# Kernel tuning notes

Measured on AMD Instinct MI355X. Metric: run time of the kernel, lower is better.

Reference implementation:

```python
import jax, jax.numpy as jnp
import numpy as np

D = 1024           # fusion_dim
H_MHA = 16         # fusion_heads
H_GAT = 8          # graph attention heads
GAT_DH = D // H_GAT
DIL = (1, 2, 4, 8, 16)
K = 7              # temporal_kernel_size
B, T = 8, 256


def setup_inputs() -> dict:
    key = jax.random.key(0)
    ks = jax.random.split(key, 20)

    def w(k, sh, fan):
        return jax.random.normal(k, sh, jnp.float32) * np.float32(1.0 / np.sqrt(fan))

    inp = {"features": jax.random.normal(ks[0], (B, T, D), jnp.float32)}
    for i, dil in enumerate(DIL):
        inp["conv_w%d" % i] = w(ks[1 + i], (D, D, K), D * K)   # torch Conv1d (out, in, k)
        inp["conv_b%d" % i] = jnp.zeros((D,), jnp.float32)
    inp["fp_w"] = w(ks[6], (D, 5 * D), 5 * D)                    # torch Linear (out, in)
    inp["fp_b"] = jnp.zeros((D,), jnp.float32)
    inp["ln_g"] = jnp.ones((D,), jnp.float32)
    inp["ln_b"] = jnp.zeros((D,), jnp.float32)
    inp["wq"] = w(ks[7], (D, D), D); inp["bq"] = jnp.zeros((D,), jnp.float32)
    inp["wk"] = w(ks[8], (D, D), D); inp["bk"] = jnp.zeros((D,), jnp.float32)
    inp["wv"] = w(ks[9], (D, D), D); inp["bv"] = jnp.zeros((D,), jnp.float32)
    inp["wo"] = w(ks[10], (D, D), D); inp["bo"] = jnp.zeros((D,), jnp.float32)
    inp["gat_w"] = w(ks[11], (D, D), D)
    inp["gat_b"] = jnp.zeros((D,), jnp.float32)
    # original `a` is (2*head_dim, 1) shared across heads; split into a1 (source) / a2 (target)
    inp["gat_a1"] = w(ks[12], (GAT_DH,), 2 * GAT_DH)
    inp["gat_a2"] = w(ks[13], (GAT_DH,), 2 * GAT_DH)
    return inp


def _forward(features, conv_ws, conv_bs, fp_w, fp_b, ln_g, ln_b,
             wq, bq, wk, bk, wv, bv, wo, bo, gat_w, gat_b, gat_a1, gat_a2):
    Bb, Tt, Dm = features.shape
    x = jnp.transpose(features, (0, 2, 1))                       # (B, D, T)
    feats = []
    for wgt, bias, dil in zip(conv_ws, conv_bs, DIL):
        pad = (K - 1) * dil // 2                                 # 'same' padding
        y = jax.lax.conv_general_dilated(
            x, wgt, window_strides=(1,), padding=[(pad, pad)],
            rhs_dilation=(dil,), dimension_numbers=("NCH", "OIH", "NCH"))
        feats.append(jnp.transpose(y + bias[None, :, None], (0, 2, 1)))
    ms = jnp.concatenate(feats, axis=-1)                         # (B, T, 5D)
    z = ms @ fp_w.T + fp_b                                       # (B, T, D)
    mu = jnp.mean(z, -1, keepdims=True)
    var = jnp.var(z, -1, keepdims=True)
    z = (z - mu) * jax.lax.rsqrt(var + 1e-5) * ln_g + ln_b       # LayerNorm
    z = jax.nn.gelu(z, approximate=False)
    # --- multi-head self attention (batch_first, no dropout at eval) ---
    dh = Dm // H_MHA
    q = (z @ wq.T + bq).reshape(Bb, Tt, H_MHA, dh)
    k = (z @ wk.T + bk).reshape(Bb, Tt, H_MHA, dh)
    v = (z @ wv.T + bv).reshape(Bb, Tt, H_MHA, dh)
    scores = jnp.einsum("bqhd,bkhd->bhqk", q, k) * np.float32(1.0 / np.sqrt(dh))
    attn = jax.nn.softmax(scores, axis=-1)
    ctx = jnp.einsum("bhqk,bkhd->bqhd", attn, v).reshape(Bb, Tt, Dm)
    att_out = ctx @ wo.T + bo
    # --- all-pairs graph attention over N = B*T nodes (GAT-style, a shared across heads) ---
    n = Bb * Tt
    hg = (att_out.reshape(n, Dm) @ gat_w.T + gat_b).reshape(n, H_GAT, GAT_DH)
    e1 = jnp.einsum("nhd,d->nh", hg, gat_a1)                     # a1 . h_i
    e2 = jnp.einsum("nhd,d->nh", hg, gat_a2)                     # a2 . h_j
    e = jax.nn.leaky_relu(e1[:, None, :] + e2[None, :, :], 0.2)  # (N, N, H) via broadcast
    alpha = jax.nn.softmax(e, axis=1)                            # normalize over j
    hp = jnp.einsum("ijh,jhd->ihd", alpha, hg).reshape(n, Dm)
    g = jax.nn.elu(hp).reshape(Bb, Tt, Dm)
    return g + features


def reference(features, conv_w0, conv_w1, conv_w2, conv_w3, conv_w4,
              conv_b0, conv_b1, conv_b2, conv_b3, conv_b4,
              fp_w, fp_b, ln_g, ln_b,
              wq, bq, wk, bk, wv, bv, wo, bo,
              gat_w, gat_b, gat_a1, gat_a2):
    return _forward(features,
                    (conv_w0, conv_w1, conv_w2, conv_w3, conv_w4),
                    (conv_b0, conv_b1, conv_b2, conv_b3, conv_b4),
                    fp_w, fp_b, ln_g, ln_b,
                    wq, bq, wk, bk, wv, bv, wo, bo,
                    gat_w, gat_b, gat_a1, gat_a2)
```

## Files before the change

### kernel.cpp

```cpp
#include <hip/hip_runtime.h>
#include <hip/hip_bf16.h>

typedef __bf16 bf16_t;
typedef bf16_t bf16x8 __attribute__((ext_vector_type(8)));
typedef bf16_t bf16x4v __attribute__((ext_vector_type(4)));
typedef float f32x4 __attribute__((ext_vector_type(4)));

__device__ __forceinline__ void gll16(const bf16_t* g, bf16_t* l) {
    __builtin_amdgcn_global_load_lds(
        (const __attribute__((address_space(1))) unsigned int*)g,
        (__attribute__((address_space(3))) unsigned int*)l, 16, 0, 0);
}

__global__ __launch_bounds__(256)
void cvt_f32_bf16(const float* __restrict__ in, bf16_t* __restrict__ out, int n4)
{
    int i = blockIdx.x * 256 + threadIdx.x;
    if (i < n4) {
        float4 v = ((const float4*)in)[i];
        bf16x4v o = { (bf16_t)v.x, (bf16_t)v.y, (bf16_t)v.z, (bf16_t)v.w };
        *(bf16x4v*)&out[i * 4] = o;
    }
}

__global__ __launch_bounds__(256)
void cvt_multi(const float* __restrict__ fpw, const float* __restrict__ wq,
               const float* __restrict__ wk, const float* __restrict__ wv,
               const float* __restrict__ wo, const float* __restrict__ gw,
               bf16_t* __restrict__ fpwb, bf16_t* __restrict__ wqb,
               bf16_t* __restrict__ wkb, bf16_t* __restrict__ wvb,
               bf16_t* __restrict__ wob, bf16_t* __restrict__ gwb)
{
    int id = blockIdx.x * 256 + threadIdx.x;
    const float* src; bf16_t* dst; int off;
    if (id < 1310720) { src = fpw; dst = fpwb; off = id; }
    else {
        int id3 = id - 1310720;
        int w = id3 >> 18; off = id3 & 262143;
        const float* ss[5] = {wq, wk, wv, wo, gw};
        bf16_t* dd[5] = {wqb, wkb, wvb, wob, gwb};
        src = ss[w]; dst = dd[w];
    }
    float4 v = ((const float4*)src)[off];
    bf16x4v o = { (bf16_t)v.x, (bf16_t)v.y, (bf16_t)v.z, (bf16_t)v.w };
    *(bf16x4v*)&dst[off * 4] = o;
}

__global__ __launch_bounds__(256)
void reorder_convw(const float* w0, const float* w1, const float* w2,
                   const float* w3, const float* w4, bf16_t* __restrict__ out)
{
    int gid = blockIdx.x * 256 + threadIdx.x;
    int i = gid >> 20, rem = gid & 1048575;
    int o = rem >> 10, c = rem & 1023;
    const float* ws[5] = {w0, w1, w2, w3, w4};
    const float* src = ws[i] + (size_t)o * 7168 + c * 7;
    #pragma unroll
    for (int kk = 0; kk < 7; kk++)
        out[((size_t)(i * 7 + kk) << 20) + (o << 10) + c] = (bf16_t)src[kk];
}

__global__ __launch_bounds__(256)
void gather_bias(const float* b0, const float* b1, const float* b2,
                 const float* b3, const float* b4,
                 const float* bq, const float* bk,
                 float* __restrict__ out, float* __restrict__ qkbias,
                 bf16_t* __restrict__ zp)
{
    int idx = blockIdx.x * 256 + threadIdx.x;
    if (blockIdx.x == 0 && threadIdx.x < 32) zp[threadIdx.x] = (bf16_t)0.0f;
    if (idx < 5120) {
        const float* bs[5] = {b0, b1, b2, b3, b4};
        out[idx] = bs[idx >> 10][idx & 1023];
    } else {
        int j = idx - 5120;
        qkbias[j] = (j < 1024) ? bq[j] : bk[j - 1024];
    }
}

template<bool CONV, bool OUT_BF16, bool BIAS_ROW = false, int NR = 128>
__global__ __launch_bounds__(256)
void mfma_gemm(const bf16_t* __restrict__ A, const bf16_t* __restrict__ Bw,
               const float* __restrict__ bias, void* __restrict__ outv,
               const bf16_t* __restrict__ zp,
               int Kd, int lda, int ldb, int ldo, int out_col0)
{
    constexpr int FN = NR / 32;
    __shared__ __align__(16) bf16_t As[3][NR * 32];
    __shared__ __align__(16) bf16_t Bs[3][128 * 32];
    const int t = threadIdx.x;
    const int lane = t & 63, wave = t >> 6;
    const int wn = (wave & 1) * (NR / 2), wm = (wave >> 1) * 64;
    const int q = lane >> 4, lr = lane & 15;
    const int mt = CONV ? (blockIdx.x & 7) : blockIdx.x;
    const int conv_i = CONV ? (blockIdx.x >> 3) : 0;
    const int m0 = mt * 128, n0 = blockIdx.y * NR;
    const int srow = lane >> 2, sseg = lane & 3;
    const int sw_seg = sseg ^ ((srow >> 1) & 3);
    const int slotq = (q ^ ((lr >> 1) & 3)) * 8;

    f32x4 acc[FN][4];
    #pragma unroll
    for (int a = 0; a < FN; a++)
        #pragma unroll
        for (int b = 0; b < 4; b++) acc[a][b] = (f32x4){0.f, 0.f, 0.f, 0.f};

    const int ksteps = Kd >> 5;
    const int T = CONV ? ksteps * 7 : ksteps;

    int s_tap = 0, s_k0 = 0;
    auto do_stage = [&](int bi) {
        const bf16_t* Bp = CONV ? (Bw + ((size_t)(conv_i * 7 + s_tap) << 20)) : Bw;
        const int shift = CONV ? ((s_tap - 3) << conv_i) : 0;
        #pragma unroll
        for (int p = 0; p < NR / 64; p++) {
            const int slab = p * 64 + wave * 16;
            const int rr = slab + srow;
            const bf16_t* ga;
            if (CONV) {
                int n = n0 + rr;
                int tg = (n & 255) + shift;
                ga = ((unsigned)tg < 256u)
                   ? A + (size_t)((n & ~255) + tg) * lda + s_k0 + sw_seg * 8
                   : zp + sseg * 8;
            } else {
                ga = A + (size_t)(n0 + rr) * lda + s_k0 + sw_seg * 8;
            }
            gll16(ga, &As[bi][slab * 32]);
        }
        #pragma unroll
        for (int p = 0; p < 2; p++) {
            const int slab = p * 64 + wave * 16;
            const int rr = slab + srow;
            gll16(Bp + (size_t)(m0 + rr) * ldb + s_k0 + sw_seg * 8, &Bs[bi][slab * 32]);
        }
        s_k0 += 32;
        if (CONV && s_k0 == Kd) { s_k0 = 0; s_tap++; }
    };

    do_stage(0);
    do_stage(1);

    int cur = 0;
    for (int s = 0; s < T; s++) {
        if (s + 1 < T) {
            if constexpr (NR == 128) asm volatile("s_waitcnt vmcnt(4)" ::: "memory");
            else                     asm volatile("s_waitcnt vmcnt(3)" ::: "memory");
        } else {
            asm volatile("s_waitcnt vmcnt(0)" ::: "memory");
        }
        __builtin_amdgcn_s_barrier();
        __builtin_amdgcn_sched_barrier(0);

        bf16x8 af[FN], bfv[4];
        #pragma unroll
        for (int f = 0; f < FN; f++)
            af[f] = *(bf16x8*)&As[cur][(wn + f * 16 + lr) * 32 + slotq];
        #pragma unroll
        for (int f = 0; f < 4; f++)
            bfv[f] = *(bf16x8*)&Bs[cur][(wm + f * 16 + lr) * 32 + slotq];

        int nb = cur + 2; if (nb >= 3) nb -= 3;
        if (s + 2 < T) do_stage(nb);

        __builtin_amdgcn_s_setprio(1);
        #pragma unroll
        for (int fn = 0; fn < FN; fn++)
            #pragma unroll
            for (int fm = 0; fm < 4; fm++)
                acc[fn][fm] = __builtin_amdgcn_mfma_f32_16x16x32_bf16(
                    af[fn], bfv[fm], acc[fn][fm], 0, 0, 0);
        __builtin_amdgcn_s_setprio(0);
        cur++; if (cur == 3) cur = 0;
    }

    const int oc0 = CONV ? (conv_i << 10) : out_col0;
    #pragma unroll
    for (int fn = 0; fn < FN; fn++) {
        #pragma unroll
        for (int r = 0; r < 4; r++) {
            int n = n0 + wn + fn * 16 + q * 4 + r;
            #pragma unroll
            for (int fm = 0; fm < 4; fm++) {
                int m = m0 + wm + fm * 16 + lr;
                float v = acc[fn][fm][r];
                if (bias) v += bias[BIAS_ROW ? n : (oc0 + m)];
                if (OUT_BF16)
                    ((bf16_t*)outv)[(size_t)n * ldo + oc0 + m] = (bf16_t)v;
                else
                    ((float*)outv)[(size_t)n * ldo + oc0 + m] = v;
            }
        }
    }
}

__global__ __launch_bounds__(256)
void ln_gelu(float* __restrict__ z, bf16_t* __restrict__ zb,
             const float* __restrict__ g, const float* __restrict__ b)
{
    __shared__ float r1[256], r2[256];
    const int n = blockIdx.x, t = threadIdx.x;
    float* row = z + (size_t)n * 1024;
    float x[4], s = 0.f, s2 = 0.f;
    #pragma unroll
    for (int u = 0; u < 4; u++) {
        x[u] = row[t + u * 256];
        s += x[u]; s2 += x[u] * x[u];
    }
    r1[t] = s; r2[t] = s2;
    __syncthreads();
    for (int off = 128; off > 0; off >>= 1) {
        if (t < off) { r1[t] += r1[t + off]; r2[t] += r2[t + off]; }
        __syncthreads();
    }
    const float mu  = r1[0] * (1.0f / 1024.0f);
    const float var = r2[0] * (1.0f / 1024.0f) - mu * mu;
    const float rstd = rsqrtf(var + 1e-5f);
    #pragma unroll
    for (int u = 0; u < 4; u++) {
        int c = t + u * 256;
        float y = (x[u] - mu) * rstd * g[c] + b[c];
        float gv = 0.5f * y * (1.0f + erff(y * 0.70710678118654752f));
        row[c] = gv;
        zb[(size_t)n * 1024 + c] = (bf16_t)gv;
    }
}

__global__ __launch_bounds__(256)
void attn_mfma(const bf16_t* __restrict__ qg, const bf16_t* __restrict__ kg,
               const bf16_t* __restrict__ vt, bf16_t* __restrict__ ctx)
{
    const int it = blockIdx.x, h = blockIdx.y, bb = blockIdx.z;
    const int t = threadIdx.x, lane = t & 63, wave = t >> 6;
    const int q4 = lane >> 4, lr = lane & 15;
    const size_t qkbase = (size_t)bb * 256 * 2048 + (size_t)h * 64;

    __shared__ __align__(16) bf16_t Qs[4][32 * 64];
    __shared__ __align__(16) bf16_t Ks[64 * 64];
    __shared__ __align__(16) bf16_t Vs[64 * 64];
    __shared__ __align__(16) bf16_t Ps[4][32 * 64];

    {
        const int itbase = it * 128;
        #pragma unroll
        for (int rep = 0; rep < 4; rep++) {
            int idx = rep * 256 + t;
            int rl = idx >> 3, seg = idx & 7;
            bf16x8 v = *(const bf16x8*)&qg[qkbase + (size_t)(itbase + rl) * 2048 + seg * 8];
            *(bf16x8*)&Qs[rl >> 5][(rl & 31) * 64 + ((seg ^ (rl & 7)) << 3)] = v;
        }
    }

    f32x4 o[2][4];
    float mrow[2][4], lrow[2][4];
    #pragma unroll
    for (int fn = 0; fn < 2; fn++)
        #pragma unroll
        for (int x = 0; x < 4; x++) {
            o[fn][x] = (f32x4){0.f, 0.f, 0.f, 0.f};
            mrow[fn][x] = -1e30f; lrow[fn][x] = 0.f;
        }

    for (int j0 = 0; j0 < 256; j0 += 64) {
        __syncthreads();
        #pragma unroll
        for (int rep = 0; rep < 2; rep++) {
            int idx = rep * 256 + t;
            int rl = idx >> 3, seg = idx & 7;
            bf16x8 kv = *(const bf16x8*)&kg[qkbase + (size_t)(j0 + rl) * 2048 + seg * 8];
            *(bf16x8*)&Ks[rl * 64 + ((seg ^ (rl & 7)) << 3)] = kv;
            bf16x8 vv = *(const bf16x8*)&vt[(size_t)(h * 64 + rl) * 2048 + bb * 256 + j0 + seg * 8];
            *(bf16x8*)&Vs[rl * 64 + ((seg ^ (rl & 7)) << 3)] = vv;
        }
        __syncthreads();

        f32x4 s[2][4];
        #pragma unroll
        for (int fn = 0; fn < 2; fn++)
            #pragma unroll
            for (int fm = 0; fm < 4; fm++) s[fn][fm] = (f32x4){0.f, 0.f, 0.f, 0.f};
        #pragma unroll
        for (int kk = 0; kk < 2; kk++) {
            bf16x8 aq[2], bk[4];
            #pragma unroll
            for (int fn = 0; fn < 2; fn++) {
                int row = fn * 16 + lr;
                aq[fn] = *(bf16x8*)&Qs[wave][row * 64 + (((kk * 4 + q4) ^ (row & 7)) << 3)];
            }
            #pragma unroll
            for (int fm = 0; fm < 4; fm++) {
                int row = fm * 16 + lr;
                bk[fm] = *(bf16x8*)&Ks[row * 64 + (((kk * 4 + q4) ^ (row & 7)) << 3)];
            }
            #pragma unroll
            for (int fn = 0; fn < 2; fn++)
                #pragma unroll
                for (int fm = 0; fm < 4; fm++)
                    s[fn][fm] = __builtin_amdgcn_mfma_f32_16x16x32_bf16(
                        aq[fn], bk[fm], s[fn][fm], 0, 0, 0);
        }

        #pragma unroll
        for (int fn = 0; fn < 2; fn++) {
            #pragma unroll
            for (int r = 0; r < 4; r++) {
                float sv[4];
                #pragma unroll
                for (int fm = 0; fm < 4; fm++) sv[fm] = s[fn][fm][r] * 0.125f;
                float rm = fmaxf(fmaxf(sv[0], sv[1]), fmaxf(sv[2], sv[3]));
                rm = fmaxf(rm, __shfl_xor(rm, 1));
                rm = fmaxf(rm, __shfl_xor(rm, 2));
                rm = fmaxf(rm, __shfl_xor(rm, 4));
                rm = fmaxf(rm, __shfl_xor(rm, 8));
                float mold = mrow[fn][r];
                float mnew = fmaxf(mold, rm);
                float scl = __expf(mold - mnew);
                mrow[fn][r] = mnew;
                int prow = fn * 16 + q4 * 4 + r;
                float psum = 0.f;
                #pragma unroll
                for (int fm = 0; fm < 4; fm++) {
                    float p = __expf(sv[fm] - mnew);
                    psum += p;
                    int col = fm * 16 + lr;
                    Ps[wave][prow * 64 + (col ^ ((prow & 7) << 3))] = (bf16_t)p;
                }
                psum += __shfl_xor(psum, 1);
                psum += __shfl_xor(psum, 2);
                psum += __shfl_xor(psum, 4);
                psum += __shfl_xor(psum, 8);
                lrow[fn][r] = lrow[fn][r] * scl + psum;
                #pragma unroll
                for (int fd = 0; fd < 4; fd++) o[fn][fd][r] *= scl;
            }
        }

        #pragma unroll
        for (int kk = 0; kk < 2; kk++) {
            bf16x8 ap[2], bvf[4];
            #pragma unroll
            for (int fn = 0; fn < 2; fn++) {
                int row = fn * 16 + lr;
                ap[fn] = *(bf16x8*)&Ps[wave][row * 64 + (((kk * 4 + q4) ^ (row & 7)) << 3)];
            }
            #pragma unroll
            for (int fd = 0; fd < 4; fd++) {
                int row = fd * 16 + lr;
                bvf[fd] = *(bf16x8*)&Vs[row * 64 + (((kk * 4 + q4) ^ (row & 7)) << 3)];
            }
            #pragma unroll
            for (int fn = 0; fn < 2; fn++)
                #pragma unroll
                for (int fd = 0; fd < 4; fd++)
                    o[fn][fd] = __builtin_amdgcn_mfma_f32_16x16x32_bf16(
                        ap[fn], bvf[fd], o[fn][fd], 0, 0, 0);
        }
    }

    const int i0 = it * 128 + wave * 32;
    #pragma unroll
    for (int fn = 0; fn < 2; fn++) {
        #pragma unroll
        for (int r = 0; r < 4; r++) {
            float inv = 1.0f / lrow[fn][r];
            int row = i0 + fn * 16 + q4 * 4 + r;
            #pragma unroll
            for (int fd = 0; fd < 4; fd++) {
                int col = h * 64 + fd * 16 + lr;
                ctx[(size_t)bb * 262144 + (size_t)row * 1024 + col] =
                    (bf16_t)(o[fn][fd][r] * inv);
            }
        }
    }
}

__global__ __launch_bounds__(256)
void gat_e(const float* __restrict__ hg, const float* __restrict__ a1,
           const float* __restrict__ a2, float* __restrict__ e1t,
           float* __restrict__ e2t)
{
    int id = blockIdx.x * 256 + threadIdx.x;
    int h = id >> 11, n = id & 2047;
    const float* hr = hg + (size_t)n * 1024 + h * 128;
    float s1 = 0.f, s2 = 0.f;
    for (int d = 0; d < 128; d += 4) {
        float4 x = *(const float4*)&hr[d];
        float4 u1 = *(const float4*)&a1[d];
        float4 u2 = *(const float4*)&a2[d];
        s1 += x.x * u1.x + x.y * u1.y + x.z * u1.z + x.w * u1.w;
        s2 += x.x * u2.x + x.y * u2.y + x.z * u2.z + x.w * u2.w;
    }
    e1t[id] = s1; e2t[id] = s2;
}

__global__ __launch_bounds__(256)
void transpose_hg(const float* __restrict__ in, bf16_t* __restrict__ out)
{
    __shared__ float tile[32][33];
    const int t = threadIdx.x;
    const int j0 = blockIdx.x * 32, c0 = blockIdx.y * 32;
    {
        int jl = t >> 3, cl = (t & 7) * 4;
        float4 v = *(const float4*)(in + (size_t)(j0 + jl) * 1024 + c0 + cl);
        tile[jl][cl] = v.x; tile[jl][cl + 1] = v.y;
        tile[jl][cl + 2] = v.z; tile[jl][cl + 3] = v.w;
    }
    __syncthreads();
    {
        int cl = t >> 3, jl = (t & 7) * 4;
        bf16x4v o = { (bf16_t)tile[jl][cl], (bf16_t)tile[jl + 1][cl],
                      (bf16_t)tile[jl + 2][cl], (bf16_t)tile[jl + 3][cl] };
        *(bf16x4v*)&out[(size_t)(c0 + cl) * 2048 + j0 + jl] = o;
    }
}

__global__ __launch_bounds__(256)
void gat_agg_mfma(const bf16_t* __restrict__ hgT, const float* __restrict__ e1t,
                  const float* __restrict__ e2t, const float* __restrict__ feat,
                  float* __restrict__ outp)
{
    const int it = blockIdx.x, h = blockIdx.y;
    const int i0 = it * 64;
    __shared__ float e2s[2048];
    __shared__ float e1s[64], mS[64], lSinv[64];
    __shared__ float pm[256], pl[256];
    __shared__ __align__(16) bf16_t Ps[64 * 136];
    __shared__ __align__(16) bf16_t Hs[128 * 136];
    const int t = threadIdx.x;
    const int lane = t & 63, wave = t >> 6;
    const int q = lane >> 4, lr = lane & 15;
    const int wm = wave * 32;

    for (int idx = t; idx < 2048; idx += 256) e2s[idx] = e2t[h * 2048 + idx];
    if (t < 64) e1s[t] = e1t[h * 2048 + i0 + t];
    __syncthreads();

    {
        int il = t & 63, jt = t >> 6;
        float ev = e1s[il];
        float m = -1e30f, l = 0.f;
        for (int j = jt; j < 2048; j += 4) {
            float x = ev + e2s[j];
            x = (x >= 0.f) ? x : 0.2f * x;
            if (x > m) { l = l * __expf(m - x) + 1.0f; m = x; }
            else       { l += __expf(x - m); }
        }
        pm[t] = m; pl[t] = l;
        __syncthreads();
        if (t < 64) {
            float M = pm[t], L = pl[t];
            #pragma unroll
            for (int g2 = 1; g2 < 4; g2++) {
                float m2 = pm[g2 * 64 + t], l2 = pl[g2 * 64 + t];
                if (m2 > M) { L = L * __expf(M - m2) + l2; M = m2; }
                else        { L += l2 * __expf(m2 - M); }
            }
            mS[t] = M; lSinv[t] = 1.0f / L;
        }
        __syncthreads();
    }

    f32x4 acc[4][2];
    #pragma unroll
    for (int a = 0; a < 4; a++)
        #pragma unroll
        for (int b = 0; b < 2; b++) acc[a][b] = (f32x4){0.f, 0.f, 0.f, 0.f};

    for (int j0 = 0; j0 < 2048; j0 += 128) {
        for (int idx = t; idx < 2048; idx += 256) {
            int d = idx >> 4, seg = idx & 15;
            *(bf16x8*)&Hs[d * 136 + seg * 8] =
                *(const bf16x8*)&hgT[(size_t)(h * 128 + d) * 2048 + j0 + seg * 8];
        }
        for (int idx = t; idx < 1024; idx += 256) {
            int i = idx >> 4, jg = idx & 15;
            float ei = e1s[i], mi = mS[i];
            bf16x8 pv;
            #pragma unroll
            for (int u = 0; u < 8; u++) {
                float x = ei + e2s[j0 + jg * 8 + u];
                x = (x >= 0.f) ? x : 0.2f * x;
                pv[u] = (bf16_t)__expf(x - mi);
            }
            *(bf16x8*)&Ps[i * 136 + jg * 8] = pv;
        }
        __syncthreads();
        #pragma unroll
        for (int kb = 0; kb < 4; kb++) {
            bf16x8 af[4], bf2[2];
            #pragma unroll
            for (int fn = 0; fn < 4; fn++)
                af[fn] = *(bf16x8*)&Ps[(fn * 16 + lr) * 136 + kb * 32 + q * 8];
            #pragma unroll
            for (int fm = 0; fm < 2; fm++)
                bf2[fm] = *(bf16x8*)&Hs[(wm + fm * 16 + lr) * 136 + kb * 32 + q * 8];
            #pragma unroll
            for (int fn = 0; fn < 4; fn++)
                #pragma unroll
                for (int fm = 0; fm < 2; fm++)
                    acc[fn][fm] = __builtin_amdgcn_mfma_f32_16x16x32_bf16(
                        af[fn], bf2[fm], acc[fn][fm], 0, 0, 0);
        }
        __syncthreads();
    }

    #pragma unroll
    for (int fn = 0; fn < 4; fn++) {
        #pragma unroll
        for (int r = 0; r < 4; r++) {
            int il = fn * 16 + q * 4 + r;
            int i = i0 + il;
            float inv = lSinv[il];
            #pragma unroll
            for (int fm = 0; fm < 2; fm++) {
                int col = h * 128 + wm + fm * 16 + lr;
                float v = acc[fn][fm][r] * inv;
                v = (v > 0.f) ? v : (expf(v) - 1.0f);
                size_t off = (size_t)i * 1024 + col;
                outp[off] = v + feat[off];
            }
        }
    }
}

extern "C" void kernel_launch(void* const* d_in, const int* in_sizes, int n_in,
                              void* d_out, int out_size, void* d_ws, size_t ws_size,
                              hipStream_t stream)
{
    const float* feat = (const float*)d_in[0];
    const float *cw[5], *cb[5];
    if (in_sizes[2] == 1024) {
        for (int i = 0; i < 5; i++) { cw[i] = (const float*)d_in[1 + 2*i]; cb[i] = (const float*)d_in[2 + 2*i]; }
    } else {
        for (int i = 0; i < 5; i++) { cw[i] = (const float*)d_in[1 + i];   cb[i] = (const float*)d_in[6 + i]; }
    }
    const float* fp_w = (const float*)d_in[11];
    const float* fp_b = (const float*)d_in[12];
    const float* ln_g = (const float*)d_in[13];
    const float* ln_b = (const float*)d_in[14];
    const float* wq = (const float*)d_in[15]; const float* bq = (const float*)d_in[16];
    const float* wk = (const float*)d_in[17]; const float* bk = (const float*)d_in[18];
    const float* wv = (const float*)d_in[19]; const float* bv = (const float*)d_in[20];
    const float* wo = (const float*)d_in[21]; const float* bo = (const float*)d_in[22];
    const float* gat_w = (const float*)d_in[23]; const float* gat_b = (const float*)d_in[24];
    const float* ga1 = (const float*)d_in[25]; const float* ga2 = (const float*)d_in[26];
    float* outp = (float*)d_out;

    char* wsb = (char*)d_ws;
    bf16_t* xb    = (bf16_t*)(wsb);
    bf16_t* msb   = (bf16_t*)(wsb + 4194304);
    bf16_t* wcb   = (bf16_t*)(wsb + 25165824);
    float*  zf    = (float*) (wsb + 98566144);
    bf16_t* zb    = (bf16_t*)(wsb + 106954752);
    bf16_t* qb    = (bf16_t*)(wsb + 111149056);
    bf16_t* kb    = (bf16_t*)(wsb + 115343360);
    bf16_t* vb    = (bf16_t*)(wsb + 119537664);
    float*  cball = (float*) (wsb + 123731968);
    float*  e1t   = (float*) (wsb + 123752448);
    float*  e2t   = (float*) (wsb + 123817984);
    bf16_t* zpage = (bf16_t*)(wsb + 123883520);
    bf16_t* fpwb = wcb;
    bf16_t* wqb  = wcb + 5242880;
    bf16_t* wkb  = wqb + 1048576;
    bf16_t* wvb  = wkb + 1048576;
    bf16_t* wob  = wvb + 1048576;
    bf16_t* gwb  = wob + 1048576;
    bf16_t* qkb  = qb;
    float*  qkbias = e1t;
    bf16_t* ctxb = zb;
    bf16_t* attb = kb;
    float*  hgb  = zf;
    bf16_t* hgtb = msb;

    const dim3 blk(256);

    cvt_f32_bf16<<<dim3(2048), blk, 0, stream>>>(feat, xb, 524288);
    reorder_convw<<<dim3(20480), blk, 0, stream>>>(cw[0], cw[1], cw[2], cw[3], cw[4], wcb);
    gather_bias<<<dim3(28), blk, 0, stream>>>(cb[0], cb[1], cb[2], cb[3], cb[4],
                                              bq, bk, cball, qkbias, zpage);

    mfma_gemm<true, true><<<dim3(40, 16), blk, 0, stream>>>(
        xb, wcb, cball, msb, zpage, 1024, 1024, 1024, 5120, 0);

    cvt_multi<<<dim3(10240), blk, 0, stream>>>(fp_w, wq, wk, wv, wo, gat_w,
                                               fpwb, wqb, wkb, wvb, wob, gwb);

    mfma_gemm<false, false, false, 64><<<dim3(8, 32), blk, 0, stream>>>(
        msb, fpwb, fp_b, zf, zpage, 5120, 5120, 5120, 1024, 0);

    ln_gelu<<<dim3(2048), blk, 0, stream>>>(zf, zb, ln_g, ln_b);

    mfma_gemm<false, true><<<dim3(16, 16), blk, 0, stream>>>(
        zb, wqb, qkbias, qkb, zpage, 1024, 1024, 1024, 2048, 0);
    mfma_gemm<false, true, true, 64><<<dim3(16, 16), blk, 0, stream>>>(
        wvb, zb, bv, vb, zpage, 1024, 1024, 1024, 2048, 0);

    attn_mfma<<<dim3(2, 16, 8), blk, 0, stream>>>(qkb, qkb + 1024, vb, ctxb);

    mfma_gemm<false, true, false, 64><<<dim3(8, 32), blk, 0, stream>>>(
        ctxb, wob, bo, attb, zpage, 1024, 1024, 1024, 1024, 0);

    mfma_gemm<false, false, false, 64><<<dim3(8, 32), blk, 0, stream>>>(
        attb, gwb, gat_b, hgb, zpage, 1024, 1024, 1024, 1024, 0);

    transpose_hg<<<dim3(64, 32), blk, 0, stream>>>(hgb, hgtb);
    gat_e<<<dim3(64), blk, 0, stream>>>(hgb, ga1, ga2, e1t, e2t);
    gat_agg_mfma<<<dim3(32, 8), blk, 0, stream>>>(hgtb, e1t, e2t, feat, outp);
}
```

Measured before the change: 709.6 us.

## Deepen GEMM pipeline to four stages, vectorize weight reorder, simplify GAT softmax

The MFMA GEMM moves from three to four LDS stages, prefetching three k-steps ahead with adjusted vmcnt waits to hide more global-load latency, at the cost of more shared memory per block. The conv A-tile address calculation gets a fast path for slabs that stay inside one sequence segment. The conv weight reorder now writes four contiguous bf16 values per thread. The GAT aggregation replaces its online max/sum pre-pass over all j with a closed-form row max from the global max of e2 (valid because leaky_relu is monotonic) and accumulates the softmax denominator during the main loop, removing a full pass over the N×N scores.

```diff
diff --git a/kernel.cpp b/kernel.cpp
--- a/kernel.cpp
+++ b/kernel.cpp
@@ -51,13 +51,15 @@
                    const float* w3, const float* w4, bf16_t* __restrict__ out)
 {
     int gid = blockIdx.x * 256 + threadIdx.x;
-    int i = gid >> 20, rem = gid & 1048575;
-    int o = rem >> 10, c = rem & 1023;
+    int i = gid / 1835008;
+    int w = gid - i * 1835008;
+    int o = w / 1792;
+    int r2 = w - o * 1792;
+    int kk = r2 >> 8, c4 = (r2 & 255) * 4;
     const float* ws[5] = {w0, w1, w2, w3, w4};
-    const float* src = ws[i] + (size_t)o * 7168 + c * 7;
-    #pragma unroll
-    for (int kk = 0; kk < 7; kk++)
-        out[((size_t)(i * 7 + kk) << 20) + (o << 10) + c] = (bf16_t)src[kk];
+    const float* src = ws[i] + (size_t)o * 7168 + c4 * 7 + kk;
+    bf16x4v v = { (bf16_t)src[0], (bf16_t)src[7], (bf16_t)src[14], (bf16_t)src[21] };
+    *(bf16x4v*)&out[((size_t)(i * 7 + kk) << 20) + (o << 10) + c4] = v;
 }
 
 __global__ __launch_bounds__(256)
@@ -86,8 +88,8 @@
                int Kd, int lda, int ldb, int ldo, int out_col0)
 {
     constexpr int FN = NR / 32;
-    __shared__ __align__(16) bf16_t As[3][NR * 32];
-    __shared__ __align__(16) bf16_t Bs[3][128 * 32];
+    __shared__ __align__(16) bf16_t As[4][NR * 32];
+    __shared__ __align__(16) bf16_t Bs[4][128 * 32];
     const int t = threadIdx.x;
     const int lane = t & 63, wave = t >> 6;
     const int wn = (wave & 1) * (NR / 2), wm = (wave >> 1) * 64;
@@ -115,16 +117,21 @@
         #pragma unroll
         for (int p = 0; p < NR / 64; p++) {
             const int slab = p * 64 + wave * 16;
-            const int rr = slab + srow;
             const bf16_t* ga;
             if (CONV) {
-                int n = n0 + rr;
-                int tg = (n & 255) + shift;
-                ga = ((unsigned)tg < 256u)
-                   ? A + (size_t)((n & ~255) + tg) * lda + s_k0 + sw_seg * 8
-                   : zp + sseg * 8;
+                const int slabN = n0 + slab;
+                const int inSeg = slabN & 255;
+                if (inSeg + shift >= 0 && inSeg + shift <= 240) {
+                    ga = A + (size_t)(slabN + srow + shift) * lda + s_k0 + sw_seg * 8;
+                } else {
+                    int n = slabN + srow;
+                    int tg = (n & 255) + shift;
+                    ga = ((unsigned)tg < 256u)
+                       ? A + (size_t)((n & ~255) + tg) * lda + s_k0 + sw_seg * 8
+                       : zp + sseg * 8;
+                }
             } else {
-                ga = A + (size_t)(n0 + rr) * lda + s_k0 + sw_seg * 8;
+                ga = A + (size_t)(n0 + slab + srow) * lda + s_k0 + sw_seg * 8;
             }
             gll16(ga, &As[bi][slab * 32]);
         }
@@ -140,10 +147,14 @@
 
     do_stage(0);
     do_stage(1);
+    do_stage(2);
 
     int cur = 0;
     for (int s = 0; s < T; s++) {
-        if (s + 1 < T) {
+        if (s + 2 < T) {
+            if constexpr (NR == 128) asm volatile("s_waitcnt vmcnt(8)" ::: "memory");
+            else                     asm volatile("s_waitcnt vmcnt(6)" ::: "memory");
+        } else if (s + 1 < T) {
             if constexpr (NR == 128) asm volatile("s_waitcnt vmcnt(4)" ::: "memory");
             else                     asm volatile("s_waitcnt vmcnt(3)" ::: "memory");
         } else {
@@ -160,8 +171,8 @@
         for (int f = 0; f < 4; f++)
             bfv[f] = *(bf16x8*)&Bs[cur][(wm + f * 16 + lr) * 32 + slotq];
 
-        int nb = cur + 2; if (nb >= 3) nb -= 3;
-        if (s + 2 < T) do_stage(nb);
+        int nb = (cur + 3) & 3;
+        if (s + 3 < T) do_stage(nb);
 
         __builtin_amdgcn_s_setprio(1);
         #pragma unroll
@@ -171,7 +182,7 @@
                 acc[fn][fm] = __builtin_amdgcn_mfma_f32_16x16x32_bf16(
                     af[fn], bfv[fm], acc[fn][fm], 0, 0, 0);
         __builtin_amdgcn_s_setprio(0);
-        cur++; if (cur == 3) cur = 0;
+        cur = (cur + 1) & 3;
     }
 
     const int oc0 = CONV ? (conv_i << 10) : out_col0;
@@ -423,7 +434,7 @@
     const int i0 = it * 64;
     __shared__ float e2s[2048];
     __shared__ float e1s[64], mS[64], lSinv[64];
-    __shared__ float pm[256], pl[256];
+    __shared__ float wmax[4];
     __shared__ __align__(16) bf16_t Ps[64 * 136];
     __shared__ __align__(16) bf16_t Hs[128 * 136];
     const int t = threadIdx.x;
@@ -431,40 +442,32 @@
     const int q = lane >> 4, lr = lane & 15;
     const int wm = wave * 32;
 
-    for (int idx = t; idx < 2048; idx += 256) e2s[idx] = e2t[h * 2048 + idx];
+    float lmax = -1e30f;
+    for (int idx = t; idx < 2048; idx += 256) {
+        float v = e2t[h * 2048 + idx];
+        e2s[idx] = v;
+        lmax = fmaxf(lmax, v);
+    }
     if (t < 64) e1s[t] = e1t[h * 2048 + i0 + t];
+    #pragma unroll
+    for (int d = 1; d < 64; d <<= 1) lmax = fmaxf(lmax, __shfl_xor(lmax, d));
+    if (lane == 0) wmax[wave] = lmax;
     __syncthreads();
-
     {
-        int il = t & 63, jt = t >> 6;
-        float ev = e1s[il];
-        float m = -1e30f, l = 0.f;
-        for (int j = jt; j < 2048; j += 4) {
-            float x = ev + e2s[j];
-            x = (x >= 0.f) ? x : 0.2f * x;
-            if (x > m) { l = l * __expf(m - x) + 1.0f; m = x; }
-            else       { l += __expf(x - m); }
-        }
-        pm[t] = m; pl[t] = l;
-        __syncthreads();
+        float maxE2 = fmaxf(fmaxf(wmax[0], wmax[1]), fmaxf(wmax[2], wmax[3]));
         if (t < 64) {
-            float M = pm[t], L = pl[t];
-            #pragma unroll
-            for (int g2 = 1; g2 < 4; g2++) {
-                float m2 = pm[g2 * 64 + t], l2 = pl[g2 * 64 + t];
-                if (m2 > M) { L = L * __expf(M - m2) + l2; M = m2; }
-                else        { L += l2 * __expf(m2 - M); }
-            }
-            mS[t] = M; lSinv[t] = 1.0f / L;
-        }
-        __syncthreads();
-    }
+            float x = e1s[t] + maxE2;
+            mS[t] = (x >= 0.f) ? x : 0.2f * x;
+        }
+    }
+    __syncthreads();
 
     f32x4 acc[4][2];
     #pragma unroll
     for (int a = 0; a < 4; a++)
         #pragma unroll
         for (int b = 0; b < 2; b++) acc[a][b] = (f32x4){0.f, 0.f, 0.f, 0.f};
+    float psum[4] = {0.f, 0.f, 0.f, 0.f};
 
     for (int j0 = 0; j0 < 2048; j0 += 128) {
         for (int idx = t; idx < 2048; idx += 256) {
@@ -472,7 +475,9 @@
             *(bf16x8*)&Hs[d * 136 + seg * 8] =
                 *(const bf16x8*)&hgT[(size_t)(h * 128 + d) * 2048 + j0 + seg * 8];
         }
-        for (int idx = t; idx < 1024; idx += 256) {
+        #pragma unroll
+        for (int rep = 0; rep < 4; rep++) {
+            int idx = rep * 256 + t;
             int i = idx >> 4, jg = idx & 15;
             float ei = e1s[i], mi = mS[i];
             bf16x8 pv;
@@ -480,7 +485,9 @@
             for (int u = 0; u < 8; u++) {
                 float x = ei + e2s[j0 + jg * 8 + u];
                 x = (x >= 0.f) ? x : 0.2f * x;
-                pv[u] = (bf16_t)__expf(x - mi);
+                float p = __expf(x - mi);
+                psum[rep] += p;
+                pv[u] = (bf16_t)p;
             }
             *(bf16x8*)&Ps[i * 136 + jg * 8] = pv;
         }
@@ -503,6 +510,17 @@
         }
         __syncthreads();
     }
+
+    #pragma unroll
+    for (int rep = 0; rep < 4; rep++) {
+        float v = psum[rep];
+        v += __shfl_xor(v, 1);
+        v += __shfl_xor(v, 2);
+        v += __shfl_xor(v, 4);
+        v += __shfl_xor(v, 8);
+        if ((t & 15) == 0) lSinv[rep * 16 + (t >> 4)] = 1.0f / v;
+    }
+    __syncthreads();
 
     #pragma unroll
     for (int fn = 0; fn < 4; fn++) {
@@ -575,7 +593,7 @@
     const dim3 blk(256);
 
     cvt_f32_bf16<<<dim3(2048), blk, 0, stream>>>(feat, xb, 524288);
-    reorder_convw<<<dim3(20480), blk, 0, stream>>>(cw[0], cw[1], cw[2], cw[3], cw[4], wcb);
+    reorder_convw<<<dim3(35840), blk, 0, stream>>>(cw[0], cw[1], cw[2], cw[3], cw[4], wcb);
     gather_bias<<<dim3(28), blk, 0, stream>>>(cb[0], cb[1], cb[2], cb[3], cb[4],
                                               bq, bk, cball, qkbias, zpage);
 
```

New measurement: 832.0 us. 17.2% more time.
